# Optimization experiments

Hardware: AMD Instinct MI355X
Metric: run time of the kernel (lower is better)

The kernel has to match this reference:

```python
import jax, jax.numpy as jnp
import numpy as np

SEQ, B = 1024, 16384

def setup_inputs() -> dict:
    key = jax.random.key(0)
    ks = jax.random.split(key, 8)
    inputs = jax.random.normal(ks[0], (SEQ, B, 1), dtype=jnp.float32)
    returns = jax.random.uniform(ks[1], (SEQ - 1, B, 1), dtype=jnp.float32) * 0.02 - 0.01
    target = jax.random.uniform(ks[2], (1,), dtype=jnp.float32)  # pi_bar (no-trade region center)
    w_in = jax.random.normal(ks[3], (1, 1), dtype=jnp.float32)   # rnn.input_param.weight (1x1)
    w_h = jax.random.normal(ks[4], (1, 1), dtype=jnp.float32)    # rnn.hidden_param.weight (1x1)
    b_h = jax.random.normal(ks[5], (1, 1), dtype=jnp.float32)    # rnn.hidden_param.bias (1x1)
    w_fc1 = jax.random.normal(ks[6], (1, 1), dtype=jnp.float32)  # rnn.fc1_param.weight (1x1)
    w_fc2 = jax.random.normal(ks[7], (1, 1), dtype=jnp.float32)  # rnn.fc2_param.weight (1x1)
    return {"inputs": inputs, "returns": returns, "target": target,
            "w_in": w_in, "w_h": w_h, "b_h": b_h, "w_fc1": w_fc1, "w_fc2": w_fc2}


def reference(inputs, returns, target, w_in, w_h, b_h, w_fc1, w_fc2):
    # inputs: [S, B, 1], returns: [S-1, B, 1]; hidden_size == 1 so per-step state h: [B, 1]
    pi_bar = target[0]

    def step(h, xr):
        x, r = xr  # x: [B,1] input at step i, r: [B,1] return at step i-1
        # wealth renormalization of previous position
        h_adj = h * (1.0 + r) / (1.0 + h * r)
        # NoTradeRegionRNN.recurrence (all params are 1x1 -> scalar broadcasts)
        ingate = x @ w_in.T + w_h * h_adj - (pi_bar - b_h)
        ingate2 = w_fc1 * jax.nn.relu(ingate) + 2.0 * b_h
        h_new = w_fc2 * jax.nn.relu(ingate2) + pi_bar + b_h
        return h_new, h_new

    h0 = inputs[0]  # i==0: hidden = input[0] * ones -> just input[0], shape [B,1]
    hT, outs = jax.lax.scan(step, h0, (inputs[1:], returns))
    output = jnp.concatenate([h0[None], outs], axis=0)  # [S, B, 1]
    return output, hT
```

## Files before the change

kernel.cpp:

```cpp
#include <hip/hip_runtime.h>
#include <cstdint>


#define S_LEN 1024
#define B_LEN 16384
#define NG    255
#define GSTEP ((size_t)4 * B_LEN)

typedef uint32_t u32x4 __attribute__((ext_vector_type(4)));
typedef float    f32x4 __attribute__((ext_vector_type(4)));
typedef float    f32x2 __attribute__((ext_vector_type(2)));

__device__ __forceinline__ u32x4 make_srsrc(const void* p) {
    u32x4 r;
    uint64_t a = (uint64_t)p;
    r.x = (uint32_t)a;
    r.y = (uint32_t)(a >> 32);
    r.z = 0xFFFFFFFFu;
    r.w = 0x00020000u;
    return r;
}

#define SBAR0 __builtin_amdgcn_sched_barrier(0)
#define WAITV(N) do { asm volatile("s_waitcnt vmcnt(%0)" :: "n"(N)); SBAR0; } while (0)
#define LGKMN(N) do { asm volatile("s_waitcnt lgkmcnt(%0)" :: "n"(N)); SBAR0; } while (0)

__device__ __forceinline__ void dma16(const float* g, float* l) {
    __builtin_amdgcn_global_load_lds(
        (const __attribute__((address_space(1))) void*)g,
        (__attribute__((address_space(3))) void*)l, 16, 0, 0);
}

__device__ __forceinline__ float step_fn(float h, float x, float r,
                                         float win, float wh,
                                         float c1, float c2, float c3,
                                         float wf1, float wf2) {
    float inv   = __builtin_amdgcn_rcpf(fmaf(h, r, 1.0f));
    float h_adj = fmaf(h, r, h) * inv;
    float ingate = fmaf(wh, h_adj, fmaf(x, win, c1));
    float t  = fmaxf(ingate, 0.0f);
    float g2 = fmaf(wf1, t, c2);
    float t2 = fmaxf(g2, 0.0f);
    return fmaf(wf2, t2, c3);
}

struct Consts {
    float winwf1, whwf1, c1wf1c2, c2p, wf2, c3;
};

template<bool POS>
__device__ __forceinline__ void step_fast(float& st, float& hv,
                                          float x, float r, const Consts& C) {
    float A1 = C.wf2 * r;
    float B1 = C.c3 * r;
    float w  = fmaf(C.whwf1, r, C.whwf1);
    float A2 = C.wf2 * w;
    float B2 = C.c3 * w;
    float KK = fmaf(x, C.winwf1, C.c1wf1c2);
    float u  = fmaf(A1, st, B1);
    float M  = fmaf(A2, st, B2);
    float q  = fmaf(u, u, 1.0f);
    float om = 1.0f - u;
    float p  = om * q;
    float Aa = fmaf(M, p, KK);
    if (POS) st = fmaxf(Aa, C.c2p);
    else     st = fminf(fmaxf(Aa, 0.0f), C.c2p);
    hv = fmaf(C.wf2, st, C.c3);
}

template<bool POS>
__device__ __forceinline__ void step_first(float& st, float& hv,
                                           float x, float r, float h0,
                                           const Consts& C) {
    float w  = fmaf(C.whwf1, r, C.whwf1);
    float KK = fmaf(x, C.winwf1, C.c1wf1c2);
    float u  = h0 * r;
    float M  = w * h0;
    float q  = fmaf(u, u, 1.0f);
    float om = 1.0f - u;
    float p  = om * q;
    float Aa = fmaf(M, p, KK);
    if (POS) st = fmaxf(Aa, C.c2p);
    else     st = fminf(fmaxf(Aa, 0.0f), C.c2p);
    hv = fmaf(C.wf2, st, C.c3);
}

#define RD_GROUP(g1, X01, X23, R01, R23) do { \
    uint32_t ax_ = rbase + (uint32_t)(((g1) & 15) * 2048); \
    uint32_t ar_ = ax_ + 1024u; \
    asm volatile("ds_read2_b32 %0, %1 offset0:0 offset1:64"    : "=v"(X01) : "v"(ax_)); \
    asm volatile("ds_read2_b32 %0, %1 offset0:128 offset1:192" : "=v"(X23) : "v"(ax_)); \
    asm volatile("ds_read2_b32 %0, %1 offset0:0 offset1:64"    : "=v"(R01) : "v"(ar_)); \
    asm volatile("ds_read2_b32 %0, %1 offset0:128 offset1:192" : "=v"(R23) : "v"(ar_)); \
} while (0)

#define WR_GROUP(g_, H0, H1, H2, H3) do { \
    uint32_t wa_ = wbase + (uint32_t)(((g_) & 7) * 1024); \
    asm volatile("ds_write2_b32 %0, %1, %2 offset0:0 offset1:64"    :: "v"(wa_), "v"(H0), "v"(H1)); \
    asm volatile("ds_write2_b32 %0, %1, %2 offset0:128 offset1:192" :: "v"(wa_), "v"(H2), "v"(H3)); \
} while (0)

#define STEPS4(X01, X23, R01, R23) do { \
    step_fast<POS>(st, hv0, (X01).x, (R01).x, C); \
    step_fast<POS>(st, hv1, (X01).y, (R01).y, C); \
    step_fast<POS>(st, hv2, (X23).x, (R23).x, C); \
    step_fast<POS>(st, hv3, (X23).y, (R23).y, C); \
} while (0)

template<bool POS>
__device__ __forceinline__ void wave0_impl(
    const float* inputs, const float* returns,
    float pi_bar, float win, float wh, float bh, float wf1, float wf2,
    float* out, int b0, int lane, float* ringp, float* outbp)
{
    const int b = b0 + lane;
    const float c1 = bh - pi_bar;
    const float c2 = 2.0f * bh;
    const float c3 = pi_bar + bh;
    Consts C;
    C.winwf1  = win * wf1;
    C.whwf1   = wh * wf1;
    C.c1wf1c2 = fmaf(c1, wf1, c2);
    C.c2p     = fmaxf(c2, 0.0f);
    C.wf2     = wf2;
    C.c3      = c3;

    const float h0v = inputs[b];
    out[b] = h0v;

    const uint32_t rbase = (uint32_t)(uintptr_t)ringp + (uint32_t)lane * 4u;
    const uint32_t wbase = (uint32_t)(uintptr_t)outbp + (uint32_t)lane * 4u;

    asm volatile("" ::: "memory");
    __builtin_amdgcn_s_barrier();

    f32x2 xA01, xA23, rA01, rA23, xB01, xB23, rB01, rB23;
    float st = 0.0f, hv0, hv1, hv2, hv3;

    RD_GROUP(0, xA01, xA23, rA01, rA23);
    LGKMN(0);

    for (int bt = 0; bt < 63; ++bt) {
        const int g0 = 4 * bt;
        RD_GROUP(g0 + 1, xB01, xB23, rB01, rB23);
        LGKMN(4);
        if (bt == 0) {
            step_first<POS>(st, hv0, xA01.x, rA01.x, h0v, C);
        } else {
            step_fast<POS>(st, hv0, xA01.x, rA01.x, C);
        }
        step_fast<POS>(st, hv1, xA01.y, rA01.y, C);
        step_fast<POS>(st, hv2, xA23.x, rA23.x, C);
        step_fast<POS>(st, hv3, xA23.y, rA23.y, C);
        WR_GROUP(g0, hv0, hv1, hv2, hv3);
        RD_GROUP(g0 + 2, xA01, xA23, rA01, rA23);
        LGKMN(6);
        STEPS4(xB01, xB23, rB01, rB23);
        WR_GROUP(g0 + 1, hv0, hv1, hv2, hv3);
        RD_GROUP(g0 + 3, xB01, xB23, rB01, rB23);
        LGKMN(6);
        STEPS4(xA01, xA23, rA01, rA23);
        WR_GROUP(g0 + 2, hv0, hv1, hv2, hv3);
        LGKMN(2);
        STEPS4(xB01, xB23, rB01, rB23);
        WR_GROUP(g0 + 3, hv0, hv1, hv2, hv3);
        RD_GROUP(g0 + 4, xA01, xA23, rA01, rA23);
        LGKMN(4);
        __builtin_amdgcn_s_barrier();
    }
    RD_GROUP(253, xB01, xB23, rB01, rB23);
    LGKMN(4);
    STEPS4(xA01, xA23, rA01, rA23);
    WR_GROUP(252, hv0, hv1, hv2, hv3);
    RD_GROUP(254, xA01, xA23, rA01, rA23);
    LGKMN(6);
    STEPS4(xB01, xB23, rB01, rB23);
    WR_GROUP(253, hv0, hv1, hv2, hv3);
    LGKMN(2);
    STEPS4(xA01, xA23, rA01, rA23);
    WR_GROUP(254, hv0, hv1, hv2, hv3);
    LGKMN(0);
    __builtin_amdgcn_s_barrier();

    asm volatile("" ::: "memory");

    float h = hv3;
#pragma unroll
    for (int s = 4 * NG + 1; s < S_LEN; ++s) {
        const float x = inputs[(size_t)s * B_LEN + b];
        const float r = returns[(size_t)(s - 1) * B_LEN + b];
        h = step_fn(h, x, r, win, wh, c1, c2, c3, wf1, wf2);
        out[(size_t)s * B_LEN + b] = h;
    }
    out[(size_t)S_LEN * B_LEN + b] = h;
}

#define W1_ITER(bt_, NDMA_, PRE_EN_, PRE_N_, O0, O1, O2, O3, END_EN_, END_N_) do { \
    for (int gi_ = 0; gi_ < (NDMA_); ++gi_) { \
        float* lb_ = &ringf[(size_t)(dmag & 15) * 512]; \
        dma16(gxw, lb_); dma16(grw, lb_ + 256); \
        gxw += GSTEP; grw += GSTEP; ++dmag; \
    } \
    if (PRE_EN_) { \
        asm volatile("s_waitcnt vmcnt(%0)" :: "n"(PRE_N_)); SBAR0; \
        asm volatile("" :: "v"(O0), "v"(O1), "v"(O2), "v"(O3)); \
    } \
    __builtin_amdgcn_s_barrier(); \
    { uint32_t a_ = oa + (uint32_t)(((bt_) & 1) * 4096); \
      asm volatile("ds_read_b128 %0, %1 offset:0"    : "=v"(O0) : "v"(a_)); \
      asm volatile("ds_read_b128 %0, %1 offset:1024" : "=v"(O1) : "v"(a_)); \
      asm volatile("ds_read_b128 %0, %1 offset:2048" : "=v"(O2) : "v"(a_)); \
      asm volatile("ds_read_b128 %0, %1 offset:3072" : "=v"(O3) : "v"(a_)); } \
    LGKMN(0); \
    { uint32_t so_ = ((uint32_t)(16 * (bt_) + 1)) << 16; \
      asm volatile("buffer_store_dwordx4 %0, %1, %2, %3 offen" :: "v"(O0), "v"(vo), "s"(ro), "s"(so_)); \
      so_ += (4u << 16); \
      asm volatile("buffer_store_dwordx4 %0, %1, %2, %3 offen" :: "v"(O1), "v"(vo), "s"(ro), "s"(so_)); \
      so_ += (4u << 16); \
      asm volatile("buffer_store_dwordx4 %0, %1, %2, %3 offen" :: "v"(O2), "v"(vo), "s"(ro), "s"(so_)); \
      so_ += (4u << 16); \
      asm volatile("buffer_store_dwordx4 %0, %1, %2, %3 offen" :: "v"(O3), "v"(vo), "s"(ro), "s"(so_)); } \
    if (END_EN_) { asm volatile("s_waitcnt vmcnt(%0)" :: "n"(END_N_)); SBAR0; } \
} while (0)

__global__ __launch_bounds__(128) void wealth_rnn_kernel(
    const float* __restrict__ inputs,
    const float* __restrict__ returns,
    const float* __restrict__ target,
    const float* __restrict__ w_in_p,
    const float* __restrict__ w_h_p,
    const float* __restrict__ b_h_p,
    const float* __restrict__ w_fc1_p,
    const float* __restrict__ w_fc2_p,
    float* __restrict__ out)
{
    __shared__ float ringf[16 * 512];
    __shared__ float outbf[8 * 256];

    const int tid  = threadIdx.x;
    const int lane = tid & 63;
    const int wid  = tid >> 6;
    const int b0   = blockIdx.x * 64;

    if (wid == 0) {
        const float pi_bar = target[0];
        const float win = w_in_p[0];
        const float wh  = w_h_p[0];
        const float bh  = b_h_p[0];
        const float wf1 = w_fc1_p[0];
        const float wf2 = w_fc2_p[0];
        if (wf1 >= 0.0f)
            wave0_impl<true >(inputs, returns, pi_bar, win, wh, bh, wf1, wf2,
                              out, b0, lane, &ringf[0], &outbf[0]);
        else
            wave0_impl<false>(inputs, returns, pi_bar, win, wh, bh, wf1, wf2,
                              out, b0, lane, &ringf[0], &outbf[0]);
    } else {
        const int j = lane;
        u32x4 ro = make_srsrc(out);
        const uint32_t vo = (uint32_t)((((j >> 4) * B_LEN) + b0 + (j & 15) * 4) * 4);
        const uint32_t oa = (uint32_t)(uintptr_t)&outbf[0]
                            + (uint32_t)((j >> 4) * 256 + (j & 15) * 16);

        const int lr = j >> 4;
        const int lc = (j & 15) * 4;
        const float* gxw = inputs  + (size_t)(1 + lr) * B_LEN + b0 + lc;
        const float* grw = returns + (size_t)lr       * B_LEN + b0 + lc;
        int dmag = 0;

        for (int gi = 0; gi < 12; ++gi) {
            float* lb_ = &ringf[(size_t)(dmag & 15) * 512];
            dma16(gxw, lb_); dma16(grw, lb_ + 256);
            gxw += GSTEP; grw += GSTEP; ++dmag;
        }
        WAITV(14);
        __builtin_amdgcn_s_barrier();

        f32x4 a0 = {0,0,0,0}, a1 = {0,0,0,0}, a2 = {0,0,0,0}, a3 = {0,0,0,0};
        f32x4 e0 = {0,0,0,0}, e1 = {0,0,0,0}, e2 = {0,0,0,0}, e3 = {0,0,0,0};

        W1_ITER(0, 4, 0, 0,  a0, a1, a2, a3, 1, 18);
        W1_ITER(1, 4, 0, 0,  e0, e1, e2, e3, 1, 22);
        for (int bt = 2; bt <= 58; bt += 2) {
            W1_ITER(bt,     4, 1, 20, a0, a1, a2, a3, 1, 22);
            W1_ITER(bt + 1, 4, 1, 20, e0, e1, e2, e3, 1, 22);
        }
        W1_ITER(60, 3, 1, 18, a0, a1, a2, a3, 1, 20);
        W1_ITER(61, 0, 1, 10, e0, e1, e2, e3, 1, 12);
        W1_ITER(62, 0, 1,  4, a0, a1, a2, a3, 1,  8);
        WAITV(4); SBAR0;
        asm volatile("" :: "v"(e0), "v"(e1), "v"(e2));
        __builtin_amdgcn_s_barrier();
        {
            uint32_t a_ = oa + 4096u;
            asm volatile("ds_read_b128 %0, %1 offset:0"    : "=v"(e0) : "v"(a_));
            asm volatile("ds_read_b128 %0, %1 offset:1024" : "=v"(e1) : "v"(a_));
            asm volatile("ds_read_b128 %0, %1 offset:2048" : "=v"(e2) : "v"(a_));
        }
        LGKMN(0);
        {
            uint32_t so_ = ((uint32_t)(16 * 63 + 1)) << 16;
            asm volatile("buffer_store_dwordx4 %0, %1, %2, %3 offen" :: "v"(e0), "v"(vo), "s"(ro), "s"(so_));
            so_ += (4u << 16);
            asm volatile("buffer_store_dwordx4 %0, %1, %2, %3 offen" :: "v"(e1), "v"(vo), "s"(ro), "s"(so_));
            so_ += (4u << 16);
            asm volatile("buffer_store_dwordx4 %0, %1, %2, %3 offen" :: "v"(e2), "v"(vo), "s"(ro), "s"(so_));
        }
    }
}

extern "C" void kernel_launch(void* const* d_in, const int* in_sizes, int n_in,
                              void* d_out, int out_size, void* d_ws, size_t ws_size,
                              hipStream_t stream) {
    const float* inputs  = (const float*)d_in[0];
    const float* returns = (const float*)d_in[1];
    const float* target  = (const float*)d_in[2];
    const float* w_in    = (const float*)d_in[3];
    const float* w_h     = (const float*)d_in[4];
    const float* b_h     = (const float*)d_in[5];
    const float* w_fc1   = (const float*)d_in[6];
    const float* w_fc2   = (const float*)d_in[7];
    float* out = (float*)d_out;

    dim3 grid(B_LEN / 64);
    dim3 block(128);
    hipLaunchKernelGGL(wealth_rnn_kernel, grid, block, 0, stream,
                       inputs, returns, target, w_in, w_h, b_h, w_fc1, w_fc2, out);
}
```

Baseline: 45.61 us.

## Double LDS ring depth and batch eight step-groups per barrier

The LDS input ring grows from 16 to 32 groups and the output staging buffer doubles. The compute wave now processes 8 groups (32 timesteps) per barrier instead of 4, using four register banks for reads. The DMA wave issues more prefetch ahead and stores 8 vectors per iteration. The goal is to halve workgroup barrier count and deepen the global-to-LDS prefetch so memory latency is hidden better. The cost is more LDS and registers, and the hand-counted waitcnt values carry more risk of error.

```diff
diff --git a/kernel.cpp b/kernel.cpp
--- a/kernel.cpp
+++ b/kernel.cpp
@@ -4,7 +4,6 @@
 
 #define S_LEN 1024
 #define B_LEN 16384
-#define NG    255
 #define GSTEP ((size_t)4 * B_LEN)
 
 typedef uint32_t u32x4 __attribute__((ext_vector_type(4)));
@@ -44,9 +43,7 @@
     return fmaf(wf2, t2, c3);
 }
 
-struct Consts {
-    float winwf1, whwf1, c1wf1c2, c2p, wf2, c3;
-};
+struct Consts { float winwf1, whwf1, c1wf1c2, c2p, wf2, c3; };
 
 template<bool POS>
 __device__ __forceinline__ void step_fast(float& st, float& hv,
@@ -85,26 +82,34 @@
     hv = fmaf(C.wf2, st, C.c3);
 }
 
-#define RD_GROUP(g1, X01, X23, R01, R23) do { \
-    uint32_t ax_ = rbase + (uint32_t)(((g1) & 15) * 2048); \
+struct Bank { f32x2 x01, x23, r01, r23; };
+
+#define RDG(g_, BK) do { \
+    uint32_t ax_ = rbase + (uint32_t)(((g_) & 31) * 2048); \
     uint32_t ar_ = ax_ + 1024u; \
-    asm volatile("ds_read2_b32 %0, %1 offset0:0 offset1:64"    : "=v"(X01) : "v"(ax_)); \
-    asm volatile("ds_read2_b32 %0, %1 offset0:128 offset1:192" : "=v"(X23) : "v"(ax_)); \
-    asm volatile("ds_read2_b32 %0, %1 offset0:0 offset1:64"    : "=v"(R01) : "v"(ar_)); \
-    asm volatile("ds_read2_b32 %0, %1 offset0:128 offset1:192" : "=v"(R23) : "v"(ar_)); \
-} while (0)
-
-#define WR_GROUP(g_, H0, H1, H2, H3) do { \
-    uint32_t wa_ = wbase + (uint32_t)(((g_) & 7) * 1024); \
-    asm volatile("ds_write2_b32 %0, %1, %2 offset0:0 offset1:64"    :: "v"(wa_), "v"(H0), "v"(H1)); \
-    asm volatile("ds_write2_b32 %0, %1, %2 offset0:128 offset1:192" :: "v"(wa_), "v"(H2), "v"(H3)); \
-} while (0)
-
-#define STEPS4(X01, X23, R01, R23) do { \
-    step_fast<POS>(st, hv0, (X01).x, (R01).x, C); \
-    step_fast<POS>(st, hv1, (X01).y, (R01).y, C); \
-    step_fast<POS>(st, hv2, (X23).x, (R23).x, C); \
-    step_fast<POS>(st, hv3, (X23).y, (R23).y, C); \
+    asm volatile("ds_read2_b32 %0, %1 offset0:0 offset1:64"    : "=v"((BK).x01) : "v"(ax_)); \
+    asm volatile("ds_read2_b32 %0, %1 offset0:128 offset1:192" : "=v"((BK).x23) : "v"(ax_)); \
+    asm volatile("ds_read2_b32 %0, %1 offset0:0 offset1:64"    : "=v"((BK).r01) : "v"(ar_)); \
+    asm volatile("ds_read2_b32 %0, %1 offset0:128 offset1:192" : "=v"((BK).r23) : "v"(ar_)); \
+} while (0)
+
+#define STEPS4B(BK) do { \
+    step_fast<POS>(st, hv0, (BK).x01.x, (BK).r01.x, C); \
+    step_fast<POS>(st, hv1, (BK).x01.y, (BK).r01.y, C); \
+    step_fast<POS>(st, hv2, (BK).x23.x, (BK).r23.x, C); \
+    step_fast<POS>(st, hv3, (BK).x23.y, (BK).r23.y, C); \
+} while (0)
+
+#define WRG(WA_) do { \
+    asm volatile("ds_write2_b32 %0, %1, %2 offset0:0 offset1:64"    :: "v"(WA_), "v"(hv0), "v"(hv1)); \
+    asm volatile("ds_write2_b32 %0, %1, %2 offset0:128 offset1:192" :: "v"(WA_), "v"(hv2), "v"(hv3)); \
+} while (0)
+
+#define PHASE(gr_, BKR, LGN_, BKC, WOFF_) do { \
+    RDG(gr_, BKR); \
+    LGKMN(LGN_); \
+    STEPS4B(BKC); \
+    { uint32_t wa_ = wb + (WOFF_); WRG(wa_); } \
 } while (0)
 
 template<bool POS>
@@ -134,59 +139,58 @@
     asm volatile("" ::: "memory");
     __builtin_amdgcn_s_barrier();
 
-    f32x2 xA01, xA23, rA01, rA23, xB01, xB23, rB01, rB23;
+    Bank B0, B1, B2, B3;
     float st = 0.0f, hv0, hv1, hv2, hv3;
 
-    RD_GROUP(0, xA01, xA23, rA01, rA23);
+    RDG(0, B0);
+    RDG(1, B1);
     LGKMN(0);
 
-    for (int bt = 0; bt < 63; ++bt) {
-        const int g0 = 4 * bt;
-        RD_GROUP(g0 + 1, xB01, xB23, rB01, rB23);
-        LGKMN(4);
-        if (bt == 0) {
-            step_first<POS>(st, hv0, xA01.x, rA01.x, h0v, C);
-        } else {
-            step_fast<POS>(st, hv0, xA01.x, rA01.x, C);
-        }
-        step_fast<POS>(st, hv1, xA01.y, rA01.y, C);
-        step_fast<POS>(st, hv2, xA23.x, rA23.x, C);
-        step_fast<POS>(st, hv3, xA23.y, rA23.y, C);
-        WR_GROUP(g0, hv0, hv1, hv2, hv3);
-        RD_GROUP(g0 + 2, xA01, xA23, rA01, rA23);
-        LGKMN(6);
-        STEPS4(xB01, xB23, rB01, rB23);
-        WR_GROUP(g0 + 1, hv0, hv1, hv2, hv3);
-        RD_GROUP(g0 + 3, xB01, xB23, rB01, rB23);
-        LGKMN(6);
-        STEPS4(xA01, xA23, rA01, rA23);
-        WR_GROUP(g0 + 2, hv0, hv1, hv2, hv3);
-        LGKMN(2);
-        STEPS4(xB01, xB23, rB01, rB23);
-        WR_GROUP(g0 + 3, hv0, hv1, hv2, hv3);
-        RD_GROUP(g0 + 4, xA01, xA23, rA01, rA23);
+    for (int bt = 0; bt < 31; ++bt) {
+        const int g0 = 8 * bt;
+        const uint32_t wb = wbase + (uint32_t)((bt & 1) << 13);
+        RDG(g0 + 2, B2);
+        LGKMN(12);
+        if (bt == 0) { step_first<POS>(st, hv0, B0.x01.x, B0.r01.x, h0v, C); }
+        else         { step_fast<POS>(st, hv0, B0.x01.x, B0.r01.x, C); }
+        step_fast<POS>(st, hv1, B0.x01.y, B0.r01.y, C);
+        step_fast<POS>(st, hv2, B0.x23.x, B0.r23.x, C);
+        step_fast<POS>(st, hv3, B0.x23.y, B0.r23.y, C);
+        { uint32_t wa_ = wb; WRG(wa_); }
+        PHASE(g0 + 3, B3, 10, B1, 1024);
+        PHASE(g0 + 4, B0, 12, B2, 2048);
+        PHASE(g0 + 5, B1, 12, B3, 3072);
+        PHASE(g0 + 6, B2, 12, B0, 4096);
+        PHASE(g0 + 7, B3, 12, B1, 5120);
+        PHASE(g0 + 8, B0, 12, B2, 6144);
+        LGKMN(8);
+        STEPS4B(B3);
+        { uint32_t wa_ = wb + 7168u; WRG(wa_); }
+        RDG(g0 + 9, B1);
         LGKMN(4);
         __builtin_amdgcn_s_barrier();
     }
-    RD_GROUP(253, xB01, xB23, rB01, rB23);
-    LGKMN(4);
-    STEPS4(xA01, xA23, rA01, rA23);
-    WR_GROUP(252, hv0, hv1, hv2, hv3);
-    RD_GROUP(254, xA01, xA23, rA01, rA23);
-    LGKMN(6);
-    STEPS4(xB01, xB23, rB01, rB23);
-    WR_GROUP(253, hv0, hv1, hv2, hv3);
-    LGKMN(2);
-    STEPS4(xA01, xA23, rA01, rA23);
-    WR_GROUP(254, hv0, hv1, hv2, hv3);
-    LGKMN(0);
-    __builtin_amdgcn_s_barrier();
+
+    {
+        const uint32_t wb = wbase + 8192u;
+        PHASE(250, B2, 12, B0, 0);
+        PHASE(251, B3, 10, B1, 1024);
+        PHASE(252, B0, 12, B2, 2048);
+        PHASE(253, B1, 12, B3, 3072);
+        PHASE(254, B2, 12, B0, 4096);
+        PHASE(254, B3, 12, B1, 5120);
+        LGKMN(8);
+        STEPS4B(B2);
+        { uint32_t wa_ = wb + 6144u; WRG(wa_); }
+        LGKMN(0);
+        __builtin_amdgcn_s_barrier();
+    }
 
     asm volatile("" ::: "memory");
 
     float h = hv3;
 #pragma unroll
-    for (int s = 4 * NG + 1; s < S_LEN; ++s) {
+    for (int s = 1021; s < S_LEN; ++s) {
         const float x = inputs[(size_t)s * B_LEN + b];
         const float r = returns[(size_t)(s - 1) * B_LEN + b];
         h = step_fn(h, x, r, win, wh, c1, c2, c3, wf1, wf2);
@@ -195,32 +199,40 @@
     out[(size_t)S_LEN * B_LEN + b] = h;
 }
 
-#define W1_ITER(bt_, NDMA_, PRE_EN_, PRE_N_, O0, O1, O2, O3, END_EN_, END_N_) do { \
-    for (int gi_ = 0; gi_ < (NDMA_); ++gi_) { \
-        float* lb_ = &ringf[(size_t)(dmag & 15) * 512]; \
-        dma16(gxw, lb_); dma16(grw, lb_ + 256); \
-        gxw += GSTEP; grw += GSTEP; ++dmag; \
-    } \
-    if (PRE_EN_) { \
-        asm volatile("s_waitcnt vmcnt(%0)" :: "n"(PRE_N_)); SBAR0; \
-        asm volatile("" :: "v"(O0), "v"(O1), "v"(O2), "v"(O3)); \
-    } \
+#define DMA_GROUP() do { \
+    float* lb_ = &ringf[(size_t)(dmag & 31) * 512]; \
+    dma16(gxw, lb_); dma16(grw, lb_ + 256); \
+    gxw += GSTEP; grw += GSTEP; ++dmag; \
+} while (0)
+
+#define WDR8(LOFF_, O0,O1,O2,O3,O4,O5,O6,O7) do { \
+    uint32_t a_ = oa + (LOFF_); \
+    asm volatile("ds_read_b128 %0, %1 offset:0"    : "=v"(O0) : "v"(a_)); \
+    asm volatile("ds_read_b128 %0, %1 offset:1024" : "=v"(O1) : "v"(a_)); \
+    asm volatile("ds_read_b128 %0, %1 offset:2048" : "=v"(O2) : "v"(a_)); \
+    asm volatile("ds_read_b128 %0, %1 offset:3072" : "=v"(O3) : "v"(a_)); \
+    asm volatile("ds_read_b128 %0, %1 offset:4096" : "=v"(O4) : "v"(a_)); \
+    asm volatile("ds_read_b128 %0, %1 offset:5120" : "=v"(O5) : "v"(a_)); \
+    asm volatile("ds_read_b128 %0, %1 offset:6144" : "=v"(O6) : "v"(a_)); \
+    asm volatile("ds_read_b128 %0, %1 offset:7168" : "=v"(O7) : "v"(a_)); \
+} while (0)
+
+#define BST(O_) do { \
+    asm volatile("buffer_store_dwordx4 %0, %1, %2, %3 offen" \
+                 :: "v"(O_), "v"(vo), "s"(ro), "s"(so_)); \
+    so_ += (4u << 16); \
+} while (0)
+
+#define W1_ITER(k_, LOFF_, NDMA_, PREN_, ENDN_, DOEND_, O0,O1,O2,O3,O4,O5,O6,O7) do { \
     __builtin_amdgcn_s_barrier(); \
-    { uint32_t a_ = oa + (uint32_t)(((bt_) & 1) * 4096); \
-      asm volatile("ds_read_b128 %0, %1 offset:0"    : "=v"(O0) : "v"(a_)); \
-      asm volatile("ds_read_b128 %0, %1 offset:1024" : "=v"(O1) : "v"(a_)); \
-      asm volatile("ds_read_b128 %0, %1 offset:2048" : "=v"(O2) : "v"(a_)); \
-      asm volatile("ds_read_b128 %0, %1 offset:3072" : "=v"(O3) : "v"(a_)); } \
+    for (int gi_ = 0; gi_ < (NDMA_); ++gi_) { DMA_GROUP(); } \
+    asm volatile("s_waitcnt vmcnt(%0)" :: "n"(PREN_)); SBAR0; \
+    asm volatile("" :: "v"(O0),"v"(O1),"v"(O2),"v"(O3),"v"(O4),"v"(O5),"v"(O6),"v"(O7)); \
+    WDR8(LOFF_, O0,O1,O2,O3,O4,O5,O6,O7); \
     LGKMN(0); \
-    { uint32_t so_ = ((uint32_t)(16 * (bt_) + 1)) << 16; \
-      asm volatile("buffer_store_dwordx4 %0, %1, %2, %3 offen" :: "v"(O0), "v"(vo), "s"(ro), "s"(so_)); \
-      so_ += (4u << 16); \
-      asm volatile("buffer_store_dwordx4 %0, %1, %2, %3 offen" :: "v"(O1), "v"(vo), "s"(ro), "s"(so_)); \
-      so_ += (4u << 16); \
-      asm volatile("buffer_store_dwordx4 %0, %1, %2, %3 offen" :: "v"(O2), "v"(vo), "s"(ro), "s"(so_)); \
-      so_ += (4u << 16); \
-      asm volatile("buffer_store_dwordx4 %0, %1, %2, %3 offen" :: "v"(O3), "v"(vo), "s"(ro), "s"(so_)); } \
-    if (END_EN_) { asm volatile("s_waitcnt vmcnt(%0)" :: "n"(END_N_)); SBAR0; } \
+    { uint32_t so_ = ((uint32_t)(32 * ((k_) - 1) + 1)) << 16; \
+      BST(O0); BST(O1); BST(O2); BST(O3); BST(O4); BST(O5); BST(O6); BST(O7); } \
+    if (DOEND_) { asm volatile("s_waitcnt vmcnt(%0)" :: "n"(ENDN_)); SBAR0; } \
 } while (0)
 
 __global__ __launch_bounds__(128) void wealth_rnn_kernel(
@@ -234,8 +246,8 @@
     const float* __restrict__ w_fc2_p,
     float* __restrict__ out)
 {
-    __shared__ float ringf[16 * 512];
-    __shared__ float outbf[8 * 256];
+    __shared__ float ringf[32 * 512];
+    __shared__ float outbf[2 * 8 * 256];
 
     const int tid  = threadIdx.x;
     const int lane = tid & 63;
@@ -268,43 +280,46 @@
         const float* grw = returns + (size_t)lr       * B_LEN + b0 + lc;
         int dmag = 0;
 
-        for (int gi = 0; gi < 12; ++gi) {
-            float* lb_ = &ringf[(size_t)(dmag & 15) * 512];
-            dma16(gxw, lb_); dma16(grw, lb_ + 256);
-            gxw += GSTEP; grw += GSTEP; ++dmag;
+        for (int gi = 0; gi < 24; ++gi) { DMA_GROUP(); }
+        WAITV(28);
+        __builtin_amdgcn_s_barrier();
+
+        for (int gi = 0; gi < 8; ++gi) { DMA_GROUP(); }
+        WAITV(28);
+
+        f32x4 o0={0,0,0,0},o1={0,0,0,0},o2={0,0,0,0},o3={0,0,0,0},
+              o4={0,0,0,0},o5={0,0,0,0},o6={0,0,0,0},o7={0,0,0,0};
+        f32x4 p0={0,0,0,0},p1={0,0,0,0},p2={0,0,0,0},p3={0,0,0,0},
+              p4={0,0,0,0},p5={0,0,0,0},p6={0,0,0,0},p7={0,0,0,0};
+
+        for (int k2 = 0; k2 < 13; ++k2) {
+            const int k = 1 + 2 * k2;
+            W1_ITER(k,     0,    8, 40, 36, 1, o0,o1,o2,o3,o4,o5,o6,o7);
+            W1_ITER(k + 1, 8192, 8, 40, 36, 1, p0,p1,p2,p3,p4,p5,p6,p7);
         }
-        WAITV(14);
+        W1_ITER(27, 0,    8, 40, 36, 1, o0,o1,o2,o3,o4,o5,o6,o7);
+        W1_ITER(28, 8192, 7, 38, 34, 1, p0,p1,p2,p3,p4,p5,p6,p7);
+        W1_ITER(29, 0,    0, 22, 18, 1, o0,o1,o2,o3,o4,o5,o6,o7);
+        W1_ITER(30, 8192, 0,  8, 16, 1, p0,p1,p2,p3,p4,p5,p6,p7);
+        W1_ITER(31, 0,    0,  8,  0, 0, o0,o1,o2,o3,o4,o5,o6,o7);
         __builtin_amdgcn_s_barrier();
 
-        f32x4 a0 = {0,0,0,0}, a1 = {0,0,0,0}, a2 = {0,0,0,0}, a3 = {0,0,0,0};
-        f32x4 e0 = {0,0,0,0}, e1 = {0,0,0,0}, e2 = {0,0,0,0}, e3 = {0,0,0,0};
-
-        W1_ITER(0, 4, 0, 0,  a0, a1, a2, a3, 1, 18);
-        W1_ITER(1, 4, 0, 0,  e0, e1, e2, e3, 1, 22);
-        for (int bt = 2; bt <= 58; bt += 2) {
-            W1_ITER(bt,     4, 1, 20, a0, a1, a2, a3, 1, 22);
-            W1_ITER(bt + 1, 4, 1, 20, e0, e1, e2, e3, 1, 22);
-        }
-        W1_ITER(60, 3, 1, 18, a0, a1, a2, a3, 1, 20);
-        W1_ITER(61, 0, 1, 10, e0, e1, e2, e3, 1, 12);
-        W1_ITER(62, 0, 1,  4, a0, a1, a2, a3, 1,  8);
-        WAITV(4); SBAR0;
-        asm volatile("" :: "v"(e0), "v"(e1), "v"(e2));
-        __builtin_amdgcn_s_barrier();
+        WAITV(8);
+        asm volatile("" :: "v"(p0),"v"(p1),"v"(p2),"v"(p3),"v"(p4),"v"(p5),"v"(p6));
         {
-            uint32_t a_ = oa + 4096u;
-            asm volatile("ds_read_b128 %0, %1 offset:0"    : "=v"(e0) : "v"(a_));
-            asm volatile("ds_read_b128 %0, %1 offset:1024" : "=v"(e1) : "v"(a_));
-            asm volatile("ds_read_b128 %0, %1 offset:2048" : "=v"(e2) : "v"(a_));
+            uint32_t a_ = oa + 8192u;
+            asm volatile("ds_read_b128 %0, %1 offset:0"    : "=v"(p0) : "v"(a_));
+            asm volatile("ds_read_b128 %0, %1 offset:1024" : "=v"(p1) : "v"(a_));
+            asm volatile("ds_read_b128 %0, %1 offset:2048" : "=v"(p2) : "v"(a_));
+            asm volatile("ds_read_b128 %0, %1 offset:3072" : "=v"(p3) : "v"(a_));
+            asm volatile("ds_read_b128 %0, %1 offset:4096" : "=v"(p4) : "v"(a_));
+            asm volatile("ds_read_b128 %0, %1 offset:5120" : "=v"(p5) : "v"(a_));
+            asm volatile("ds_read_b128 %0, %1 offset:6144" : "=v"(p6) : "v"(a_));
         }
         LGKMN(0);
         {
-            uint32_t so_ = ((uint32_t)(16 * 63 + 1)) << 16;
-            asm volatile("buffer_store_dwordx4 %0, %1, %2, %3 offen" :: "v"(e0), "v"(vo), "s"(ro), "s"(so_));
-            so_ += (4u << 16);
-            asm volatile("buffer_store_dwordx4 %0, %1, %2, %3 offen" :: "v"(e1), "v"(vo), "s"(ro), "s"(so_));
-            so_ += (4u << 16);
-            asm volatile("buffer_store_dwordx4 %0, %1, %2, %3 offen" :: "v"(e2), "v"(vo), "s"(ro), "s"(so_));
+            uint32_t so_ = ((uint32_t)993) << 16;
+            BST(p0); BST(p1); BST(p2); BST(p3); BST(p4); BST(p5); BST(p6);
         }
     }
 }
```

Result: faster. 43.69 us (-4.2%).
